# Optimization experiments

Hardware: AMD Instinct MI355X
Metric: run time of the kernel (lower is better)

Reference implementation:

```python
import jax, jax.numpy as jnp
import numpy as np

B, N, D, H = 8, 2048, 256, 8
HD = D // H  # head_dim = 32
LN_EPS = 1e-5


def setup_inputs() -> dict:
    key = jax.random.key(0)
    ks = jax.random.split(key, 8)
    x = jax.random.normal(ks[0], (B, N, D), dtype=jnp.float32)
    # dense 0/1 adjacency with guaranteed self-loops (avoids all -inf softmax rows)
    adj = jax.random.randint(ks[1], (B, N, N), 0, 2, dtype=jnp.int32)
    adj = jnp.maximum(adj, jnp.eye(N, dtype=jnp.int32)[None, :, :])
    s = 0.02
    Wq = jax.random.normal(ks[2], (D, D), dtype=jnp.float32) * s
    Wk = jax.random.normal(ks[3], (D, D), dtype=jnp.float32) * s
    Wv = jax.random.normal(ks[4], (D, D), dtype=jnp.float32) * s
    Wo = jax.random.normal(ks[5], (D, D), dtype=jnp.float32) * s
    zeros = jnp.zeros((D,), dtype=jnp.float32)
    return {
        "x": x, "adjacency": adj,
        "Wq": Wq, "bq": zeros, "Wk": Wk, "bk": zeros,
        "Wv": Wv, "bv": zeros, "Wo": Wo, "bo": zeros,
        "gamma": jnp.ones((D,), dtype=jnp.float32), "beta": zeros,
    }


def reference(x, adjacency, Wq, bq, Wk, bk, Wv, bv, Wo, bo, gamma, beta):
    b, n, d = x.shape
    q = (x @ Wq + bq).reshape(b, n, H, HD)
    k = (x @ Wk + bk).reshape(b, n, H, HD)
    v = (x @ Wv + bv).reshape(b, n, H, HD)
    # scores: [B, N(query), M(key), H]
    scores = jnp.einsum('bnhd,bmhd->bnmh', q, k) / jnp.sqrt(jnp.float32(HD))
    mask = (adjacency == 0)[..., None]  # [B,N,M,1] broadcasts over heads
    scores = jnp.where(mask, -jnp.inf, scores)
    weights = jax.nn.softmax(scores, axis=2)  # softmax over key axis m
    # dropout is identity in eval mode
    attended = jnp.einsum('bnmh,bmhd->bnhd', weights, v).reshape(b, n, d)
    out = attended @ Wo + bo
    out = out + x  # residual (output.shape == x.shape since input_dim == output_dim)
    mu = jnp.mean(out, axis=-1, keepdims=True)
    var = jnp.mean(jnp.square(out - mu), axis=-1, keepdims=True)
    return (out - mu) * jax.lax.rsqrt(var + LN_EPS) * gamma + beta
```

## Files before the change

### kernel.cpp

```cpp
#include <hip/hip_runtime.h>
#include <hip/hip_bf16.h>
#include <cstdint>
#include <cstddef>

#define B_ 8
#define N_ 2048
#define D_ 256
#define H_ 8
#define HD_ 32
#define LN_EPS 1e-5f
#define QSCALE 0.25506275f

typedef __attribute__((ext_vector_type(8))) short short8;
typedef __attribute__((ext_vector_type(4))) float f32x4;
typedef __attribute__((ext_vector_type(16))) float f32x16;

static __device__ __forceinline__ float exp2v(float x) {
#if __has_builtin(__builtin_amdgcn_exp2f)
    return __builtin_amdgcn_exp2f(x);
#else
    float r;
    asm("v_exp_f32 %0, %1" : "=v"(r) : "v"(x));
    return r;
#endif
}

static __device__ __forceinline__ unsigned short f2bf(float f) {
    union { float f; unsigned int u; } v; v.f = f;
    unsigned int r = v.u + 0x7fffu + ((v.u >> 16) & 1u);
    return (unsigned short)(r >> 16);
}

static __device__ __forceinline__ unsigned int cvtpk(float lo, float hi) {
    unsigned int d;
    asm("v_cvt_pk_bf16_f32 %0, %1, %2" : "=v"(d) : "v"(lo), "v"(hi));
    return d;
}

__global__ __launch_bounds__(256) void k_prep_w(const float* __restrict__ w0, const float* __restrict__ w1,
                                                const float* __restrict__ w2, const float* __restrict__ w3,
                                                unsigned short* __restrict__ wt) {
    int c = blockIdx.x, mat = blockIdx.y, k = threadIdx.x;
    const float* w = (mat == 0) ? w0 : (mat == 1) ? w1 : (mat == 2) ? w2 : w3;
    wt[((size_t)(mat * 256 + c)) * 256 + k] = f2bf(w[k * 256 + c]);
}

__global__ __launch_bounds__(256) void k_mask(const int* __restrict__ adj,
                                              unsigned int* __restrict__ mbg) {
    int wave = (blockIdx.x * 256 + threadIdx.x) >> 6;
    int lane = threadIdx.x & 63;
    int shamt = 4 * (lane & 7);
    int g8 = lane >> 3;
    const int4* p = reinterpret_cast<const int4*>(adj) + (size_t)wave * 512 + lane;
    unsigned int* outp = mbg + (size_t)wave * 64;

    int4 v[8];
#pragma unroll
    for (int i = 0; i < 8; ++i)
        v[i] = p[i * 64];
    __builtin_amdgcn_sched_barrier(0);

#pragma unroll
    for (int i = 0; i < 8; ++i) {
        unsigned int nib = (v[i].x != 0 ? 1u : 0u) | (v[i].y != 0 ? 2u : 0u)
                         | (v[i].z != 0 ? 4u : 0u) | (v[i].w != 0 ? 8u : 0u);
        unsigned int r = nib << shamt;
        r |= (unsigned int)__shfl_xor((int)r, 1, 64);
        r |= (unsigned int)__shfl_xor((int)r, 2, 64);
        r |= (unsigned int)__shfl_xor((int)r, 4, 64);
        if ((lane & 7) == 0) outp[i * 8 + g8] = r;
    }
}

__global__ __launch_bounds__(256) void k_qkv(const float* __restrict__ x,
                                             const unsigned short* __restrict__ wt,
                                             const float* __restrict__ bq, const float* __restrict__ bk,
                                             const float* __restrict__ bv,
                                             unsigned short* __restrict__ Qb, unsigned short* __restrict__ Kb,
                                             unsigned short* __restrict__ Vs) {
    int mat = blockIdx.y;
    int lane = threadIdx.x & 63;
    int wv = threadIdx.x >> 6;
    int row0 = blockIdx.x * 64 + wv * 16;
    int l15 = lane & 15, lg = lane >> 4;
    const float* bias = (mat == 0) ? bq : (mat == 1) ? bk : bv;
    const float qs = (mat == 0) ? QSCALE : 1.0f;
    const unsigned short* wm = wt + (size_t)mat * 65536;

    short8 af[8];
    const float* xrow = x + (size_t)(row0 + l15) * 256 + lg * 8;
#pragma unroll
    for (int kk = 0; kk < 8; ++kk) {
        float4 a = *reinterpret_cast<const float4*>(xrow + kk * 32);
        float4 b = *reinterpret_cast<const float4*>(xrow + kk * 32 + 4);
        union { short8 s8; unsigned int u[4]; } t;
        t.u[0] = cvtpk(a.x, a.y); t.u[1] = cvtpk(a.z, a.w);
        t.u[2] = cvtpk(b.x, b.y); t.u[3] = cvtpk(b.z, b.w);
        af[kk] = t.s8;
    }

    int b = row0 >> 11;
    int nbase = (row0 & 2047) + lg * 4;

    for (int ci = 0; ci < 16; ++ci) {
        const unsigned short* wrow = wm + (size_t)(ci * 16 + l15) * 256 + lg * 8;
        f32x4 acc = {0.f, 0.f, 0.f, 0.f};
#pragma unroll
        for (int kk = 0; kk < 8; ++kk) {
            short8 bfg = *reinterpret_cast<const short8*>(wrow + kk * 32);
            acc = __builtin_amdgcn_mfma_f32_16x16x32_bf16(af[kk], bfg, acc, 0, 0, 0);
        }
        int col = ci * 16 + l15;
        float bcol = bias[col];
        int h = col >> 5, hd = col & 31;
        if (mat < 2) {
            unsigned short* dst = (mat == 0) ? Qb : Kb;
#pragma unroll
            for (int r = 0; r < 4; ++r) {
                size_t off = ((size_t)(b * 8 + h) * 2048 + nbase + r) * 32 + hd;
                dst[off] = f2bf((acc[r] + bcol) * qs);
            }
        } else {
            size_t off = (size_t)(b * 8 + h) * 65536
                       + ((size_t)(nbase >> 4) * 32 + hd) * 16 + (nbase & 15);
            ushort4 o;
            o.x = f2bf(acc[0] + bcol); o.y = f2bf(acc[1] + bcol);
            o.z = f2bf(acc[2] + bcol); o.w = f2bf(acc[3] + bcol);
            *reinterpret_cast<ushort4*>(Vs + off) = o;
        }
    }
}

__global__ __launch_bounds__(256, 6) void k_attn(const unsigned short* __restrict__ Qb,
                                                 const unsigned short* __restrict__ Kb,
                                                 const unsigned short* __restrict__ Vs,
                                                 const unsigned int* __restrict__ mbg,
                                                 unsigned short* __restrict__ att) {
    __shared__ unsigned int mbits[32][66];
    int tid = threadIdx.x;
    int lane = tid & 63;
    int l31 = lane & 31, hi = lane >> 5;
    int b = blockIdx.x & 7;
    int hg = (blockIdx.x >> 3) & 1;
    int q0 = (blockIdx.x >> 4) * 32;
    int head = hg * 4 + (tid >> 6);

    {
        int row = tid >> 3, c0 = (tid & 7) * 8;
        const unsigned int* src = mbg + ((size_t)(b * N_ + q0 + row)) * 64 + c0;
        uint4 v4 = *reinterpret_cast<const uint4*>(src);
        uint4 w4 = *reinterpret_cast<const uint4*>(src + 4);
        mbits[row][c0 + 0] = v4.x; mbits[row][c0 + 1] = v4.y;
        mbits[row][c0 + 2] = v4.z; mbits[row][c0 + 3] = v4.w;
        mbits[row][c0 + 4] = w4.x; mbits[row][c0 + 5] = w4.y;
        mbits[row][c0 + 6] = w4.z; mbits[row][c0 + 7] = w4.w;
    }
    __syncthreads();

    int bh = b * 8 + head;
    const unsigned short* Qh = Qb + (size_t)bh * N_ * HD_;
    const unsigned short* Kh = Kb + (size_t)bh * N_ * HD_;
    const unsigned short* Vh = Vs + (size_t)bh * 65536;

    short8 qf0 = *reinterpret_cast<const short8*>(Qh + (size_t)(q0 + l31) * HD_ + hi * 8);
    short8 qf1 = *reinterpret_cast<const short8*>(Qh + (size_t)(q0 + l31) * HD_ + hi * 8 + 16);
    const unsigned short* krow = Kh + (size_t)l31 * HD_ + hi * 8;
    const unsigned short* vfp = Vh + (size_t)l31 * 16 + hi * 8;

    const f32x16 fz = {0.f,0.f,0.f,0.f,0.f,0.f,0.f,0.f,0.f,0.f,0.f,0.f,0.f,0.f,0.f,0.f};
    const short8 onesf = {0x3F80, 0x3F80, 0x3F80, 0x3F80, 0x3F80, 0x3F80, 0x3F80, 0x3F80};
    f32x16 attacc = fz;
    f32x16 onesacc = fz;
    const unsigned int* mrow = &mbits[l31][0];

#pragma unroll 2
    for (int m0 = 0; m0 < N_; m0 += 32) {
        short8 kf0 = *reinterpret_cast<const short8*>(krow + (size_t)m0 * HD_);
        short8 kf1 = *reinterpret_cast<const short8*>(krow + (size_t)m0 * HD_ + 16);
        short8 vf0 = *reinterpret_cast<const short8*>(vfp + (size_t)(m0 >> 4) * 512);
        short8 vf1 = *reinterpret_cast<const short8*>(vfp + (size_t)(m0 >> 4) * 512 + 512);
        unsigned int wl = mrow[m0 >> 5] >> (4 * hi);

        __builtin_amdgcn_s_setprio(1);
        f32x16 s = __builtin_amdgcn_mfma_f32_32x32x16_bf16(kf0, qf0, fz, 0, 0, 0);
        s = __builtin_amdgcn_mfma_f32_32x32x16_bf16(kf1, qf1, s, 0, 0, 0);
        __builtin_amdgcn_s_setprio(0);

        unsigned int pd[4][2];
#pragma unroll
        for (int g = 0; g < 4; ++g) {
            unsigned int nib = (wl >> (8 * g)) & 15u;
            float p0 = (nib & 1u) ? exp2v(s[4 * g + 0]) : 0.f;
            float p1 = (nib & 2u) ? exp2v(s[4 * g + 1]) : 0.f;
            float p2 = (nib & 4u) ? exp2v(s[4 * g + 2]) : 0.f;
            float p3 = (nib & 8u) ? exp2v(s[4 * g + 3]) : 0.f;
            pd[g][0] = cvtpk(p0, p1);
            pd[g][1] = cvtpk(p2, p3);
        }
        asm("v_permlane32_swap_b32 %0, %1" : "+v"(pd[0][0]), "+v"(pd[1][0]));
        asm("v_permlane32_swap_b32 %0, %1" : "+v"(pd[0][1]), "+v"(pd[1][1]));
        asm("v_permlane32_swap_b32 %0, %1" : "+v"(pd[2][0]), "+v"(pd[3][0]));
        asm("v_permlane32_swap_b32 %0, %1" : "+v"(pd[2][1]), "+v"(pd[3][1]));

        union { short8 s8; unsigned int u[4]; } bf0, bf1;
        bf0.u[0] = pd[0][0]; bf0.u[1] = pd[0][1]; bf0.u[2] = pd[1][0]; bf0.u[3] = pd[1][1];
        bf1.u[0] = pd[2][0]; bf1.u[1] = pd[2][1]; bf1.u[2] = pd[3][0]; bf1.u[3] = pd[3][1];

        __builtin_amdgcn_s_setprio(1);
        attacc = __builtin_amdgcn_mfma_f32_32x32x16_bf16(vf0, bf0.s8, attacc, 0, 0, 0);
        attacc = __builtin_amdgcn_mfma_f32_32x32x16_bf16(vf1, bf1.s8, attacc, 0, 0, 0);
        onesacc = __builtin_amdgcn_mfma_f32_32x32x16_bf16(onesf, bf0.s8, onesacc, 0, 0, 0);
        onesacc = __builtin_amdgcn_mfma_f32_32x32x16_bf16(onesf, bf1.s8, onesacc, 0, 0, 0);
        __builtin_amdgcn_s_setprio(0);
    }

    float rcp = 1.f / onesacc[0];

    unsigned short* arow = att + ((size_t)b * N_ + q0 + l31) * D_ + head * HD_;
#pragma unroll
    for (int g = 0; g < 4; ++g) {
        ushort4 o;
        o.x = f2bf(attacc[4 * g + 0] * rcp);
        o.y = f2bf(attacc[4 * g + 1] * rcp);
        o.z = f2bf(attacc[4 * g + 2] * rcp);
        o.w = f2bf(attacc[4 * g + 3] * rcp);
        *reinterpret_cast<ushort4*>(arow + 8 * g + 4 * hi) = o;
    }
}

__global__ __launch_bounds__(256) void k_outln(const unsigned short* __restrict__ att,
                                               const unsigned short* __restrict__ wot,
                                               const float* __restrict__ bo,
                                               const float* __restrict__ x,
                                               const float* __restrict__ gamma, const float* __restrict__ beta,
                                               float* __restrict__ out) {
    int lane = threadIdx.x & 63, wv = threadIdx.x >> 6;
    int l15 = lane & 15, lg = lane >> 4;
    int row0 = blockIdx.x * 64 + wv * 16;

    short8 af[8];
    const unsigned short* arow = att + (size_t)(row0 + l15) * 256 + lg * 8;
#pragma unroll
    for (int kk = 0; kk < 8; ++kk)
        af[kk] = *reinterpret_cast<const short8*>(arow + kk * 32);

    float v[16][4];
#pragma unroll
    for (int ci = 0; ci < 16; ++ci) {
        const unsigned short* wrow = wot + (size_t)(ci * 16 + l15) * 256 + lg * 8;
        f32x4 acc = {0.f, 0.f, 0.f, 0.f};
#pragma unroll
        for (int kk = 0; kk < 8; ++kk) {
            short8 bfg = *reinterpret_cast<const short8*>(wrow + kk * 32);
            acc = __builtin_amdgcn_mfma_f32_16x16x32_bf16(af[kk], bfg, acc, 0, 0, 0);
        }
        float bcol = bo[ci * 16 + l15];
#pragma unroll
        for (int r = 0; r < 4; ++r)
            v[ci][r] = acc[r] + bcol + x[(size_t)(row0 + lg * 4 + r) * 256 + ci * 16 + l15];
    }

    float sum[4] = {0.f, 0.f, 0.f, 0.f}, sq[4] = {0.f, 0.f, 0.f, 0.f};
#pragma unroll
    for (int ci = 0; ci < 16; ++ci)
#pragma unroll
        for (int r = 0; r < 4; ++r) {
            sum[r] += v[ci][r];
            sq[r] += v[ci][r] * v[ci][r];
        }
#pragma unroll
    for (int d = 1; d < 16; d <<= 1)
#pragma unroll
        for (int r = 0; r < 4; ++r) {
            sum[r] += __shfl_xor(sum[r], d, 64);
            sq[r] += __shfl_xor(sq[r], d, 64);
        }

    float mu[4], rs[4];
#pragma unroll
    for (int r = 0; r < 4; ++r) {
        mu[r] = sum[r] * (1.f / 256.f);
        float var = sq[r] * (1.f / 256.f) - mu[r] * mu[r];
        rs[r] = rsqrtf(var + LN_EPS);
    }

#pragma unroll
    for (int ci = 0; ci < 16; ++ci) {
        float g = gamma[ci * 16 + l15], be = beta[ci * 16 + l15];
#pragma unroll
        for (int r = 0; r < 4; ++r)
            out[(size_t)(row0 + lg * 4 + r) * 256 + ci * 16 + l15] = (v[ci][r] - mu[r]) * rs[r] * g + be;
    }
}

extern "C" void kernel_launch(void* const* d_in, const int* in_sizes, int n_in,
                              void* d_out, int out_size, void* d_ws, size_t ws_size,
                              hipStream_t stream) {
    (void)in_sizes; (void)n_in; (void)out_size; (void)ws_size;
    const float* x     = (const float*)d_in[0];
    const int*   adj   = (const int*)d_in[1];
    const float* Wq    = (const float*)d_in[2];
    const float* bq    = (const float*)d_in[3];
    const float* Wk    = (const float*)d_in[4];
    const float* bk    = (const float*)d_in[5];
    const float* Wv    = (const float*)d_in[6];
    const float* bv    = (const float*)d_in[7];
    const float* Wo    = (const float*)d_in[8];
    const float* bo    = (const float*)d_in[9];
    const float* gamma = (const float*)d_in[10];
    const float* beta  = (const float*)d_in[11];
    float* out = (float*)d_out;

    char* ws = (char*)d_ws;
    unsigned short* wt  = (unsigned short*)ws; ws += (size_t)4 * 256 * 256 * 2;
    unsigned short* Qb  = (unsigned short*)ws; ws += (size_t)B_ * H_ * N_ * HD_ * 2;
    unsigned short* Kb  = (unsigned short*)ws; ws += (size_t)B_ * H_ * N_ * HD_ * 2;
    unsigned short* Vs  = (unsigned short*)ws; ws += (size_t)B_ * H_ * N_ * HD_ * 2;
    unsigned short* att = (unsigned short*)ws; ws += (size_t)16384 * 256 * 2;
    unsigned int*   mbg = (unsigned int*)ws;   ws += (size_t)B_ * N_ * 64 * 4;

    k_prep_w<<<dim3(256, 4), 256, 0, stream>>>(Wq, Wk, Wv, Wo, wt);
    k_mask<<<4096, 256, 0, stream>>>(adj, mbg);
    k_qkv<<<dim3(256, 3), 256, 0, stream>>>(x, wt, bq, bk, bv, Qb, Kb, Vs);
    k_attn<<<1024, 256, 0, stream>>>(Qb, Kb, Vs, mbg, att);
    k_outln<<<256, 256, 0, stream>>>(att, wt + 3 * 65536, bo, x, gamma, beta, out);
}
```

Before: 183.8 us.

## Transpose mask bits into per-lane SGPR-loadable layout and merge QKV launch

Adds a kernel that bit-transposes the packed adjacency mask so that each key-tile's mask for 32 queries becomes 64-bit lane masks. The attention loop loads these with scalar loads and applies them via v_cndmask with an SGPR lane mask, removing the LDS mask staging, the syncthreads, and the per-element nibble extraction. Exponentials are now always computed before masking. Separately, the QKV kernel loops over the three matrices inside one block instead of using a grid dimension, reusing the converted x fragments but cutting grid parallelism threefold. It adds an extra kernel launch, extra workspace, and hand-written inline asm with manual waitcnt handling.

```diff
diff --git a/kernel.cpp b/kernel.cpp
--- a/kernel.cpp
+++ b/kernel.cpp
@@ -72,20 +72,56 @@
     }
 }
 
+__global__ __launch_bounds__(256) void k_maskT2(const unsigned int* __restrict__ mbg,
+                                                unsigned int* __restrict__ mbgT2) {
+    __shared__ unsigned int bits[64][65];
+    int tid = threadIdx.x, lane = tid & 63, wv = tid >> 6;
+    int b = blockIdx.x >> 5, qg = blockIdx.x & 31;
+
+    {
+        int row = tid >> 2, cc = (tid & 3) * 16;
+        const uint4* src = reinterpret_cast<const uint4*>(
+            mbg + ((size_t)(b * N_ + qg * 64 + row)) * 64 + cc);
+#pragma unroll
+        for (int j = 0; j < 4; ++j) {
+            uint4 v = src[j];
+            bits[row][cc + 4 * j + 0] = v.x; bits[row][cc + 4 * j + 1] = v.y;
+            bits[row][cc + 4 * j + 2] = v.z; bits[row][cc + 4 * j + 3] = v.w;
+        }
+    }
+    __syncthreads();
+
+    int h = lane >> 5, l31 = lane & 31;
+    const unsigned int M[5] = {0x0000FFFFu, 0x00FF00FFu, 0x0F0F0F0Fu, 0x33333333u, 0x55555555u};
+#pragma unroll
+    for (int j = 0; j < 16; ++j) {
+        int kw = wv * 16 + j;
+        unsigned int w = bits[lane][kw];
+#pragma unroll
+        for (int si = 0; si < 5; ++si) {
+            int s = 16 >> si;
+            unsigned int m = M[si];
+            unsigned int t = (unsigned int)__shfl_xor((int)w, s, 64);
+            unsigned int a = (w & m) | ((t & m) << s);
+            unsigned int c = (w & ~m) | ((t >> s) & m);
+            w = (lane & s) ? c : a;
+        }
+        int k = kw * 32 + l31;
+        int kp = (k & ~7) | ((k & 3) << 1) | ((k >> 2) & 1);
+        mbgT2[((size_t)(b * 64 + qg * 2 + h)) * 2048 + kp] = w;
+    }
+}
+
 __global__ __launch_bounds__(256) void k_qkv(const float* __restrict__ x,
                                              const unsigned short* __restrict__ wt,
                                              const float* __restrict__ bq, const float* __restrict__ bk,
                                              const float* __restrict__ bv,
                                              unsigned short* __restrict__ Qb, unsigned short* __restrict__ Kb,
                                              unsigned short* __restrict__ Vs) {
-    int mat = blockIdx.y;
     int lane = threadIdx.x & 63;
     int wv = threadIdx.x >> 6;
     int row0 = blockIdx.x * 64 + wv * 16;
     int l15 = lane & 15, lg = lane >> 4;
-    const float* bias = (mat == 0) ? bq : (mat == 1) ? bk : bv;
-    const float qs = (mat == 0) ? QSCALE : 1.0f;
-    const unsigned short* wm = wt + (size_t)mat * 65536;
 
     short8 af[8];
     const float* xrow = x + (size_t)(row0 + l15) * 256 + lg * 8;
@@ -102,62 +138,64 @@
     int b = row0 >> 11;
     int nbase = (row0 & 2047) + lg * 4;
 
-    for (int ci = 0; ci < 16; ++ci) {
-        const unsigned short* wrow = wm + (size_t)(ci * 16 + l15) * 256 + lg * 8;
-        f32x4 acc = {0.f, 0.f, 0.f, 0.f};
-#pragma unroll
-        for (int kk = 0; kk < 8; ++kk) {
-            short8 bfg = *reinterpret_cast<const short8*>(wrow + kk * 32);
-            acc = __builtin_amdgcn_mfma_f32_16x16x32_bf16(af[kk], bfg, acc, 0, 0, 0);
-        }
-        int col = ci * 16 + l15;
-        float bcol = bias[col];
-        int h = col >> 5, hd = col & 31;
-        if (mat < 2) {
-            unsigned short* dst = (mat == 0) ? Qb : Kb;
-#pragma unroll
-            for (int r = 0; r < 4; ++r) {
-                size_t off = ((size_t)(b * 8 + h) * 2048 + nbase + r) * 32 + hd;
-                dst[off] = f2bf((acc[r] + bcol) * qs);
+#pragma unroll 1
+    for (int mat = 0; mat < 3; ++mat) {
+        const float* bias = (mat == 0) ? bq : (mat == 1) ? bk : bv;
+        const float qs = (mat == 0) ? QSCALE : 1.0f;
+        const unsigned short* wm = wt + (size_t)mat * 65536;
+        for (int ci = 0; ci < 16; ++ci) {
+            const unsigned short* wrow = wm + (size_t)(ci * 16 + l15) * 256 + lg * 8;
+            f32x4 acc = {0.f, 0.f, 0.f, 0.f};
+#pragma unroll
+            for (int kk = 0; kk < 8; ++kk) {
+                short8 bfg = *reinterpret_cast<const short8*>(wrow + kk * 32);
+                acc = __builtin_amdgcn_mfma_f32_16x16x32_bf16(af[kk], bfg, acc, 0, 0, 0);
             }
-        } else {
-            size_t off = (size_t)(b * 8 + h) * 65536
-                       + ((size_t)(nbase >> 4) * 32 + hd) * 16 + (nbase & 15);
-            ushort4 o;
-            o.x = f2bf(acc[0] + bcol); o.y = f2bf(acc[1] + bcol);
-            o.z = f2bf(acc[2] + bcol); o.w = f2bf(acc[3] + bcol);
-            *reinterpret_cast<ushort4*>(Vs + off) = o;
-        }
-    }
-}
+            int col = ci * 16 + l15;
+            float bcol = bias[col];
+            int h = col >> 5, hd = col & 31;
+            if (mat < 2) {
+                unsigned short* dst = (mat == 0) ? Qb : Kb;
+#pragma unroll
+                for (int r = 0; r < 4; ++r) {
+                    size_t off = ((size_t)(b * 8 + h) * 2048 + nbase + r) * 32 + hd;
+                    dst[off] = f2bf((acc[r] + bcol) * qs);
+                }
+            } else {
+                size_t off = (size_t)(b * 8 + h) * 65536
+                           + ((size_t)(nbase >> 4) * 32 + hd) * 16 + (nbase & 15);
+                ushort4 o;
+                o.x = f2bf(acc[0] + bcol); o.y = f2bf(acc[1] + bcol);
+                o.z = f2bf(acc[2] + bcol); o.w = f2bf(acc[3] + bcol);
+                *reinterpret_cast<ushort4*>(Vs + off) = o;
+            }
+        }
+    }
+}
+
+#define SL(j, offs) asm("s_load_dwordx2 %0, %1, " offs : "=s"(m##j) : "s"(mbase))
+#define SLOAD16() do { \
+    SL(0, "0x0");  SL(1, "0x8");  SL(2, "0x10"); SL(3, "0x18"); \
+    SL(4, "0x20"); SL(5, "0x28"); SL(6, "0x30"); SL(7, "0x38"); \
+    SL(8, "0x40"); SL(9, "0x48"); SL(10, "0x50"); SL(11, "0x58"); \
+    SL(12, "0x60"); SL(13, "0x68"); SL(14, "0x70"); SL(15, "0x78"); } while (0)
+#define CND(d, s_, mj) asm("v_cndmask_b32 %0, 0, %1, %2" : "=v"(d) : "v"(s_), "s"(mj))
 
 __global__ __launch_bounds__(256, 6) void k_attn(const unsigned short* __restrict__ Qb,
                                                  const unsigned short* __restrict__ Kb,
                                                  const unsigned short* __restrict__ Vs,
-                                                 const unsigned int* __restrict__ mbg,
+                                                 const unsigned int* __restrict__ mbgT2,
                                                  unsigned short* __restrict__ att) {
-    __shared__ unsigned int mbits[32][66];
     int tid = threadIdx.x;
     int lane = tid & 63;
     int l31 = lane & 31, hi = lane >> 5;
     int b = blockIdx.x & 7;
     int hg = (blockIdx.x >> 3) & 1;
-    int q0 = (blockIdx.x >> 4) * 32;
+    int qt32 = blockIdx.x >> 4;
+    int q0 = qt32 * 32;
     int head = hg * 4 + (tid >> 6);
-
-    {
-        int row = tid >> 3, c0 = (tid & 7) * 8;
-        const unsigned int* src = mbg + ((size_t)(b * N_ + q0 + row)) * 64 + c0;
-        uint4 v4 = *reinterpret_cast<const uint4*>(src);
-        uint4 w4 = *reinterpret_cast<const uint4*>(src + 4);
-        mbits[row][c0 + 0] = v4.x; mbits[row][c0 + 1] = v4.y;
-        mbits[row][c0 + 2] = v4.z; mbits[row][c0 + 3] = v4.w;
-        mbits[row][c0 + 4] = w4.x; mbits[row][c0 + 5] = w4.y;
-        mbits[row][c0 + 6] = w4.z; mbits[row][c0 + 7] = w4.w;
-    }
-    __syncthreads();
-
     int bh = b * 8 + head;
+
     const unsigned short* Qh = Qb + (size_t)bh * N_ * HD_;
     const unsigned short* Kh = Kb + (size_t)bh * N_ * HD_;
     const unsigned short* Vh = Vs + (size_t)bh * 65536;
@@ -167,36 +205,51 @@
     const unsigned short* krow = Kh + (size_t)l31 * HD_ + hi * 8;
     const unsigned short* vfp = Vh + (size_t)l31 * 16 + hi * 8;
 
+    unsigned long long mbase = (unsigned long long)(mbgT2 + (size_t)(b * 64 + qt32) * 2048);
+    unsigned long long m0, m1, m2, m3, m4, m5, m6, m7, m8, m9, m10, m11, m12, m13, m14, m15;
+    SLOAD16();
+
     const f32x16 fz = {0.f,0.f,0.f,0.f,0.f,0.f,0.f,0.f,0.f,0.f,0.f,0.f,0.f,0.f,0.f,0.f};
     const short8 onesf = {0x3F80, 0x3F80, 0x3F80, 0x3F80, 0x3F80, 0x3F80, 0x3F80, 0x3F80};
     f32x16 attacc = fz;
     f32x16 onesacc = fz;
-    const unsigned int* mrow = &mbits[l31][0];
 
 #pragma unroll 2
-    for (int m0 = 0; m0 < N_; m0 += 32) {
-        short8 kf0 = *reinterpret_cast<const short8*>(krow + (size_t)m0 * HD_);
-        short8 kf1 = *reinterpret_cast<const short8*>(krow + (size_t)m0 * HD_ + 16);
-        short8 vf0 = *reinterpret_cast<const short8*>(vfp + (size_t)(m0 >> 4) * 512);
-        short8 vf1 = *reinterpret_cast<const short8*>(vfp + (size_t)(m0 >> 4) * 512 + 512);
-        unsigned int wl = mrow[m0 >> 5] >> (4 * hi);
+    for (int t = 0; t < 64; ++t) {
+        short8 kf0 = *reinterpret_cast<const short8*>(krow + (size_t)t * 1024);
+        short8 kf1 = *reinterpret_cast<const short8*>(krow + (size_t)t * 1024 + 16);
+        short8 vf0 = *reinterpret_cast<const short8*>(vfp + (size_t)t * 1024);
+        short8 vf1 = *reinterpret_cast<const short8*>(vfp + (size_t)t * 1024 + 512);
 
         __builtin_amdgcn_s_setprio(1);
         f32x16 s = __builtin_amdgcn_mfma_f32_32x32x16_bf16(kf0, qf0, fz, 0, 0, 0);
         s = __builtin_amdgcn_mfma_f32_32x32x16_bf16(kf1, qf1, s, 0, 0, 0);
         __builtin_amdgcn_s_setprio(0);
 
+        float e0 = exp2v(s[0]),  e1 = exp2v(s[1]),  e2 = exp2v(s[2]),  e3 = exp2v(s[3]);
+        float e4 = exp2v(s[4]),  e5 = exp2v(s[5]),  e6 = exp2v(s[6]),  e7 = exp2v(s[7]);
+        float e8 = exp2v(s[8]),  e9 = exp2v(s[9]),  e10 = exp2v(s[10]), e11 = exp2v(s[11]);
+        float e12 = exp2v(s[12]), e13 = exp2v(s[13]), e14 = exp2v(s[14]), e15 = exp2v(s[15]);
+
+        asm volatile("s_waitcnt lgkmcnt(0)"
+                     : "+s"(m0), "+s"(m1), "+s"(m2), "+s"(m3), "+s"(m4), "+s"(m5), "+s"(m6), "+s"(m7),
+                       "+s"(m8), "+s"(m9), "+s"(m10), "+s"(m11), "+s"(m12), "+s"(m13), "+s"(m14), "+s"(m15));
+
+        float p0, p1, p2, p3, p4, p5, p6, p7, p8, p9, p10, p11, p12, p13, p14, p15;
+        CND(p0, e0, m0);   CND(p1, e1, m1);   CND(p2, e2, m2);   CND(p3, e3, m3);
+        CND(p4, e4, m4);   CND(p5, e5, m5);   CND(p6, e6, m6);   CND(p7, e7, m7);
+        CND(p8, e8, m8);   CND(p9, e9, m9);   CND(p10, e10, m10); CND(p11, e11, m11);
+        CND(p12, e12, m12); CND(p13, e13, m13); CND(p14, e14, m14); CND(p15, e15, m15);
+
         unsigned int pd[4][2];
-#pragma unroll
-        for (int g = 0; g < 4; ++g) {
-            unsigned int nib = (wl >> (8 * g)) & 15u;
-            float p0 = (nib & 1u) ? exp2v(s[4 * g + 0]) : 0.f;
-            float p1 = (nib & 2u) ? exp2v(s[4 * g + 1]) : 0.f;
-            float p2 = (nib & 4u) ? exp2v(s[4 * g + 2]) : 0.f;
-            float p3 = (nib & 8u) ? exp2v(s[4 * g + 3]) : 0.f;
-            pd[g][0] = cvtpk(p0, p1);
-            pd[g][1] = cvtpk(p2, p3);
-        }
+        pd[0][0] = cvtpk(p0, p1);   pd[0][1] = cvtpk(p2, p3);
+        pd[1][0] = cvtpk(p4, p5);   pd[1][1] = cvtpk(p6, p7);
+        pd[2][0] = cvtpk(p8, p9);   pd[2][1] = cvtpk(p10, p11);
+        pd[3][0] = cvtpk(p12, p13); pd[3][1] = cvtpk(p14, p15);
+
+        mbase += 128;
+        SLOAD16();
+
         asm("v_permlane32_swap_b32 %0, %1" : "+v"(pd[0][0]), "+v"(pd[1][0]));
         asm("v_permlane32_swap_b32 %0, %1" : "+v"(pd[0][1]), "+v"(pd[1][1]));
         asm("v_permlane32_swap_b32 %0, %1" : "+v"(pd[2][0]), "+v"(pd[3][0]));
@@ -312,16 +365,18 @@
     float* out = (float*)d_out;
 
     char* ws = (char*)d_ws;
-    unsigned short* wt  = (unsigned short*)ws; ws += (size_t)4 * 256 * 256 * 2;
-    unsigned short* Qb  = (unsigned short*)ws; ws += (size_t)B_ * H_ * N_ * HD_ * 2;
-    unsigned short* Kb  = (unsigned short*)ws; ws += (size_t)B_ * H_ * N_ * HD_ * 2;
-    unsigned short* Vs  = (unsigned short*)ws; ws += (size_t)B_ * H_ * N_ * HD_ * 2;
-    unsigned short* att = (unsigned short*)ws; ws += (size_t)16384 * 256 * 2;
-    unsigned int*   mbg = (unsigned int*)ws;   ws += (size_t)B_ * N_ * 64 * 4;
+    unsigned short* wt   = (unsigned short*)ws; ws += (size_t)4 * 256 * 256 * 2;
+    unsigned short* Qb   = (unsigned short*)ws; ws += (size_t)B_ * H_ * N_ * HD_ * 2;
+    unsigned short* Kb   = (unsigned short*)ws; ws += (size_t)B_ * H_ * N_ * HD_ * 2;
+    unsigned short* Vs   = (unsigned short*)ws; ws += (size_t)B_ * H_ * N_ * HD_ * 2;
+    unsigned short* att  = (unsigned short*)ws; ws += (size_t)16384 * 256 * 2;
+    unsigned int*   mbg  = (unsigned int*)ws;   ws += (size_t)B_ * N_ * 64 * 4;
+    unsigned int*   mbgT2 = (unsigned int*)ws;  ws += (size_t)B_ * 64 * 2048 * 4 + 256;
 
     k_prep_w<<<dim3(256, 4), 256, 0, stream>>>(Wq, Wk, Wv, Wo, wt);
     k_mask<<<4096, 256, 0, stream>>>(adj, mbg);
-    k_qkv<<<dim3(256, 3), 256, 0, stream>>>(x, wt, bq, bk, bv, Qb, Kb, Vs);
-    k_attn<<<1024, 256, 0, stream>>>(Qb, Kb, Vs, mbg, att);
+    k_maskT2<<<256, 256, 0, stream>>>(mbg, mbgT2);
+    k_qkv<<<256, 256, 0, stream>>>(x, wt, bq, bk, bv, Qb, Kb, Vs);
+    k_attn<<<1024, 256, 0, stream>>>(Qb, Kb, Vs, mbgT2, att);
     k_outln<<<256, 256, 0, stream>>>(att, wt + 3 * 65536, bo, x, gamma, beta, out);
 }
```

Result: no change. 183.3 us (-0.3%).
